# Optimization experiments

Measured on AMD Instinct MI355X. Metric: run time of the kernel, lower is better.

## Reference

```python
import jax, jax.numpy as jnp
import numpy as np

TEMPERATURE = 12.5   # args.temperature (DeepEMD default)
EPS = 0.05           # entropic regularization for the OT (EMD) solve
N_ITERS = 100        # Sinkhorn iterations
COS_EPS = 1e-8       # F.cosine_similarity eps


def setup_inputs() -> dict:
    key = jax.random.key(0)
    k1, k2 = jax.random.split(key)
    B, C, H, W = 512, 1024, 8, 8
    proto = jax.random.normal(k1, (B, C, H, W), dtype=jnp.float32)
    query = jax.random.normal(k2, (B, C, H, W), dtype=jnp.float32)
    return {"proto": proto, "query": query}


def get_weight_vector(A, Bmap):
    """A,[b,c,h,w]; pooled Bmap reweights A's channels -> node weights [b, h*w]."""
    pooled = Bmap.mean(axis=(2, 3), keepdims=True)          # adaptive_avg_pool2d -> [b,c,1,1]
    comb = (A * pooled).sum(axis=1).reshape(A.shape[0], -1)  # [b, h*w]
    return jax.nn.relu(comb) + 0.001


def center(x):
    # args.norm == 'center': subtract channel mean
    return x - x.mean(axis=1, keepdims=True)


def cosine_sim_map(proto, query):
    """sim[b, q_node, p_node] = cosine similarity between flattened spatial nodes."""
    B, C = proto.shape[0], proto.shape[1]
    p = proto.reshape(B, C, -1).transpose(0, 2, 1)   # [b, Np, c]
    q = query.reshape(B, C, -1).transpose(0, 2, 1)   # [b, Nq, c]
    pn = p / jnp.maximum(jnp.linalg.norm(p, axis=-1, keepdims=True), COS_EPS)
    qn = q / jnp.maximum(jnp.linalg.norm(q, axis=-1, keepdims=True), COS_EPS)
    return jnp.einsum('bqc,bpc->bqp', qn, pn)        # [b, Nq, Np]


def sinkhorn_flow(cost, r, c):
    """Entropic-regularized OT flow with marginals r [b,N], c [b,M]; cost [b,N,M]."""
    K = jnp.exp(-cost / EPS)
    v0 = jnp.ones_like(c)

    def body(v, _):
        u = r / jnp.maximum(jnp.einsum('bnm,bm->bn', K, v), 1e-30)
        v = c / jnp.maximum(jnp.einsum('bnm,bn->bm', K, u), 1e-30)
        return v, None

    v, _ = jax.lax.scan(body, v0, None, length=N_ITERS)
    u = r / jnp.maximum(jnp.einsum('bnm,bm->bn', K, v), 1e-30)
    return u[:, :, None] * K * v[:, None, :]         # [b, N, M]


def reference(proto, query):
    # emd_forward(proto, query)
    weight_1 = get_weight_vector(query, proto)       # [b, Nq]
    weight_2 = get_weight_vector(proto, query)       # [b, Np]
    p = center(proto)
    q = center(query)
    sim = cosine_sim_map(p, q)                       # [b, Nq, Np]
    # get_emd_distance: solve OT on cost = 1 - sim with (normalized) node weights
    r = weight_1 / weight_1.sum(axis=-1, keepdims=True)
    c = weight_2 / weight_2.sum(axis=-1, keepdims=True)
    flow = sinkhorn_flow(1.0 - sim, r, c)
    num_node = weight_1.shape[-1]
    logits = (sim * flow).sum(axis=(-1, -2)) * (TEMPERATURE / num_node)
    return logits
```

## Files before the change

### kernel.cpp

```cpp
#include <hip/hip_runtime.h>
#include <math.h>

#define NCH    1024
#define NN     64
#define CK     32
#define KSC    28.853900817779268f
#define SPLIT  4
#define WSB    4352

#define STAT_Q(v) { sqp[0]+=(v).x; q2p[0]=fmaf((v).x,(v).x,q2p[0]); \
                    sqp[1]+=(v).y; q2p[1]=fmaf((v).y,(v).y,q2p[1]); \
                    sqp[2]+=(v).z; q2p[2]=fmaf((v).z,(v).z,q2p[2]); \
                    sqp[3]+=(v).w; q2p[3]=fmaf((v).w,(v).w,q2p[3]); }
#define STAT_P(v) { spp[0]+=(v).x; p2p[0]=fmaf((v).x,(v).x,p2p[0]); \
                    spp[1]+=(v).y; p2p[1]=fmaf((v).y,(v).y,p2p[1]); \
                    spp[2]+=(v).z; p2p[2]=fmaf((v).z,(v).z,p2p[2]); \
                    spp[3]+=(v).w; p2p[3]=fmaf((v).w,(v).w,p2p[3]); }

#define GRAM_CHUNK_BODY(NCHUNK_, QB_, PB_)                                     \
    for (int ch = 0; ch < (NCHUNK_); ++ch) {                                   \
        if (ch) __syncthreads();                                               \
        *(float4*)&stage[       ofs] = qv0;                                    \
        *(float4*)&stage[1024 + ofs] = qv1;                                    \
        *(float4*)&stage[2048 + ofs] = pv0;                                    \
        *(float4*)&stage[3072 + ofs] = pv1;                                    \
        float4 nq0, nq1, np0, np1;                                             \
        const bool more = (ch + 1 < (NCHUNK_));                                \
        if (more) {                                                            \
            const float* qn = (QB_) + (ch + 1) * 2048;                         \
            const float* pn = (PB_) + (ch + 1) * 2048;                         \
            nq0 = *(const float4*)(qn + ofs);                                  \
            nq1 = *(const float4*)(qn + 1024 + ofs);                           \
            np0 = *(const float4*)(pn + ofs);                                  \
            np1 = *(const float4*)(pn + 1024 + ofs);                           \
        }                                                                      \
        STAT_Q(qv0); STAT_Q(qv1);                                              \
        STAT_P(pv0); STAT_P(pv1);                                              \
        __syncthreads();                                                       \
        _Pragma("unroll 8")                                                    \
        for (int cc = 0; cc < CK; ++cc) {                                      \
            float4 a  = *(const float4*)&stage[cc * 64 + n0];                  \
            float4 bb = *(const float4*)&stage[2048 + cc * 64 + m0];           \
            acc[0][0]=fmaf(a.x,bb.x,acc[0][0]); acc[0][1]=fmaf(a.x,bb.y,acc[0][1]); \
            acc[0][2]=fmaf(a.x,bb.z,acc[0][2]); acc[0][3]=fmaf(a.x,bb.w,acc[0][3]); \
            acc[1][0]=fmaf(a.y,bb.x,acc[1][0]); acc[1][1]=fmaf(a.y,bb.y,acc[1][1]); \
            acc[1][2]=fmaf(a.y,bb.z,acc[1][2]); acc[1][3]=fmaf(a.y,bb.w,acc[1][3]); \
            acc[2][0]=fmaf(a.z,bb.x,acc[2][0]); acc[2][1]=fmaf(a.z,bb.y,acc[2][1]); \
            acc[2][2]=fmaf(a.z,bb.z,acc[2][2]); acc[2][3]=fmaf(a.z,bb.w,acc[2][3]); \
            acc[3][0]=fmaf(a.w,bb.x,acc[3][0]); acc[3][1]=fmaf(a.w,bb.y,acc[3][1]); \
            acc[3][2]=fmaf(a.w,bb.z,acc[3][2]); acc[3][3]=fmaf(a.w,bb.w,acc[3][3]); \
        }                                                                      \
        if (more) { qv0 = nq0; qv1 = nq1; pv0 = np0; pv1 = np1; }              \
    }

#define DOT16(KK, ARR) ({ \
    float4 x0 = *(const float4*)&ARR[sp4*16 +  0]; \
    float4 x1 = *(const float4*)&ARR[sp4*16 +  4]; \
    float4 x2 = *(const float4*)&ARR[sp4*16 +  8]; \
    float4 x3 = *(const float4*)&ARR[sp4*16 + 12]; \
    float a0 = 0.0f, a1 = 0.0f; \
    a0=fmaf(KK[0],x0.x,a0);  a1=fmaf(KK[1],x0.y,a1); \
    a0=fmaf(KK[2],x0.z,a0);  a1=fmaf(KK[3],x0.w,a1); \
    a0=fmaf(KK[4],x1.x,a0);  a1=fmaf(KK[5],x1.y,a1); \
    a0=fmaf(KK[6],x1.z,a0);  a1=fmaf(KK[7],x1.w,a1); \
    a0=fmaf(KK[8],x2.x,a0);  a1=fmaf(KK[9],x2.y,a1); \
    a0=fmaf(KK[10],x2.z,a0); a1=fmaf(KK[11],x2.w,a1); \
    a0=fmaf(KK[12],x3.x,a0); a1=fmaf(KK[13],x3.y,a1); \
    a0=fmaf(KK[14],x3.z,a0); a1=fmaf(KK[15],x3.w,a1); \
    a0 + a1; })

__global__ __launch_bounds__(256)
void gram_partial(const float* __restrict__ proto,
                  const float* __restrict__ query,
                  float* __restrict__ ws)
{
    __shared__ __align__(16) float stage[4096];

    const int bid = blockIdx.x;
    const int b = bid >> 2, s = bid & (SPLIT - 1);
    const int t  = threadIdx.x;
    const int tr = t >> 4, tc = t & 15;
    const int n0 = tr * 4, m0 = tc * 4;
    const int ofs = 4 * t;

    const float* __restrict__ pb = proto + (size_t)b * (NCH * NN) + s * (NCH / SPLIT) * NN;
    const float* __restrict__ qb = query + (size_t)b * (NCH * NN) + s * (NCH / SPLIT) * NN;

    float acc[4][4];
    #pragma unroll
    for (int i = 0; i < 4; ++i)
        #pragma unroll
        for (int j = 0; j < 4; ++j) acc[i][j] = 0.0f;
    float sqp[4] = {0,0,0,0}, q2p[4] = {0,0,0,0};
    float spp[4] = {0,0,0,0}, p2p[4] = {0,0,0,0};

    float4 qv0 = *(const float4*)(qb + ofs);
    float4 qv1 = *(const float4*)(qb + 1024 + ofs);
    float4 pv0 = *(const float4*)(pb + ofs);
    float4 pv1 = *(const float4*)(pb + 1024 + ofs);

    GRAM_CHUNK_BODY(NCH / SPLIT / CK, qb, pb)
    __syncthreads();

    float* __restrict__ wsb = ws + (size_t)bid * WSB;
    #pragma unroll
    for (int i = 0; i < 4; ++i) {
        float4 v; v.x = acc[i][0]; v.y = acc[i][1]; v.z = acc[i][2]; v.w = acc[i][3];
        *(float4*)&wsb[(n0 + i) * 64 + m0] = v;
    }

    #pragma unroll
    for (int k = 0; k < 4; ++k) {
        stage[t*16 +      k] = sqp[k];
        stage[t*16 +  4 + k] = q2p[k];
        stage[t*16 +  8 + k] = spp[k];
        stage[t*16 + 12 + k] = p2p[k];
    }
    __syncthreads();
    if (t < NN) {
        const int g = t >> 2, k = t & 3;
        float ssq = 0, sq2 = 0, ssp = 0, sp2 = 0;
        #pragma unroll
        for (int j = 0; j < 16; ++j) {
            const float* row = &stage[(j * 16 + g) * 16];
            ssq += row[k]; sq2 += row[4 + k]; ssp += row[8 + k]; sp2 += row[12 + k];
        }
        wsb[4096 +   0 + t] = ssq;
        wsb[4096 +  64 + t] = sq2;
        wsb[4096 + 128 + t] = ssp;
        wsb[4096 + 192 + t] = sp2;
    }
}

__global__ __launch_bounds__(256)
void emd_solve(const float* __restrict__ ws, float* __restrict__ out)
{
    __shared__ __align__(16) float stage[16 * 64];
    __shared__ __align__(16) float Kl [NN][68];
    __shared__ __align__(16) float KTl[NN][68];
    __shared__ __align__(16) float statL[4][NN];
    __shared__ __align__(16) float uL[NN];
    __shared__ __align__(16) float vL[NN];
    __shared__ __align__(16) float rL[NN];
    __shared__ __align__(16) float cL[NN];
    __shared__ float redl[4];

    const int b  = blockIdx.x;
    const int t  = threadIdx.x;
    const int tr = t >> 4, tc = t & 15;
    const int n0 = tr * 4, m0 = tc * 4;

    const float* __restrict__ wsb = ws + (size_t)b * SPLIT * WSB;

    float acc[4][4];
    #pragma unroll
    for (int i = 0; i < 4; ++i)
        #pragma unroll
        for (int j = 0; j < 4; ++j) acc[i][j] = 0.0f;
    #pragma unroll
    for (int s = 0; s < SPLIT; ++s) {
        const float* __restrict__ g = wsb + s * WSB;
        #pragma unroll
        for (int i = 0; i < 4; ++i) {
            float4 v = *(const float4*)&g[(n0 + i) * 64 + m0];
            acc[i][0] += v.x; acc[i][1] += v.y; acc[i][2] += v.z; acc[i][3] += v.w;
        }
    }
    if (t < NN) {
        float s0 = 0, s1 = 0, s2 = 0, s3 = 0;
        #pragma unroll
        for (int s = 0; s < SPLIT; ++s) {
            const float* __restrict__ g = wsb + s * WSB + 4096;
            s0 += g[t]; s1 += g[64 + t]; s2 += g[128 + t]; s3 += g[192 + t];
        }
        statL[0][t] = s0; statL[1][t] = s1; statL[2][t] = s2; statL[3][t] = s3;
    }
    #pragma unroll
    for (int i = 0; i < 4; ++i) {
        float s = acc[i][0] + acc[i][1] + acc[i][2] + acc[i][3];
        s += __shfl_xor(s, 1, 64); s += __shfl_xor(s, 2, 64);
        s += __shfl_xor(s, 4, 64); s += __shfl_xor(s, 8, 64);
        if (tc == 0) uL[n0 + i] = s;
    }
    #pragma unroll
    for (int j = 0; j < 4; ++j)
        stage[tr * 64 + m0 + j] = acc[0][j] + acc[1][j] + acc[2][j] + acc[3][j];
    __syncthreads();

    if (t < NN) {
        float cs = 0;
        #pragma unroll
        for (int i = 0; i < 16; ++i) cs += stage[i * 64 + t];
        float w2 = fmaxf(cs * (1.0f/64.0f), 0.0f) + 0.001f;
        float w1 = fmaxf(uL[t] * (1.0f/64.0f), 0.0f) + 0.001f;
        float s1 = w1, s2 = w2;
        #pragma unroll
        for (int m = 1; m < 64; m <<= 1) {
            s1 += __shfl_xor(s1, m, 64);
            s2 += __shfl_xor(s2, m, 64);
        }
        rL[t] = w1 / s1;
        cL[t] = w2 / s2;
        vL[t] = 1.0f;
    }
    {
        float nq_[4], np_[4], sqn[4], spm[4];
        #pragma unroll
        for (int i = 0; i < 4; ++i) {
            float sv  = statL[0][n0 + i];
            float var = statL[1][n0 + i] - sv * sv * (1.0f/1024.0f);
            nq_[i] = fmaxf(sqrtf(fmaxf(var, 0.0f)), 1e-8f);
            sqn[i] = sv;
        }
        #pragma unroll
        for (int j = 0; j < 4; ++j) {
            float sv  = statL[2][m0 + j];
            float var = statL[3][m0 + j] - sv * sv * (1.0f/1024.0f);
            np_[j] = fmaxf(sqrtf(fmaxf(var, 0.0f)), 1e-8f);
            spm[j] = sv;
        }
        #pragma unroll
        for (int i = 0; i < 4; ++i) {
            #pragma unroll
            for (int j = 0; j < 4; ++j) {
                float sim = (acc[i][j] - sqn[i] * spm[j] * (1.0f/1024.0f)) / (nq_[i] * np_[j]);
                acc[i][j] = sim;
                float Kv = exp2f((sim - 1.0f) * KSC);
                Kl [n0 + i][m0 + j] = Kv;
                KTl[m0 + j][n0 + i] = Kv;
            }
        }
    }
    __syncthreads();

    const int sn  = t >> 2;
    const int sp4 = t & 3;
    float Kr[16], KTr[16];
    #pragma unroll
    for (int jj = 0; jj < 4; ++jj) {
        float4 kv = *(const float4*)&Kl [sn][sp4 * 16 + jj * 4];
        float4 kt = *(const float4*)&KTl[sn][sp4 * 16 + jj * 4];
        Kr [jj*4+0]=kv.x; Kr [jj*4+1]=kv.y; Kr [jj*4+2]=kv.z; Kr [jj*4+3]=kv.w;
        KTr[jj*4+0]=kt.x; KTr[jj*4+1]=kt.y; KTr[jj*4+2]=kt.z; KTr[jj*4+3]=kt.w;
    }
    const float rreg = rL[sn];
    const float creg = cL[sn];

    for (int it = 0; it < 100; ++it) {
        float s = DOT16(Kr, vL);
        s += __shfl_xor(s, 1, 64); s += __shfl_xor(s, 2, 64);
        float u = rreg / fmaxf(s, 1e-30f);
        if (sp4 == 0) uL[sn] = u;
        __syncthreads();
        float s2 = DOT16(KTr, uL);
        s2 += __shfl_xor(s2, 1, 64); s2 += __shfl_xor(s2, 2, 64);
        float vv = creg / fmaxf(s2, 1e-30f);
        if (sp4 == 0) vL[sn] = vv;
        __syncthreads();
    }
    {
        float s = DOT16(Kr, vL);
        s += __shfl_xor(s, 1, 64); s += __shfl_xor(s, 2, 64);
        float u = rreg / fmaxf(s, 1e-30f);
        if (sp4 == 0) uL[sn] = u;
    }
    __syncthreads();

    float uu[4], vv_[4];
    #pragma unroll
    for (int i = 0; i < 4; ++i) uu[i]  = uL[n0 + i];
    #pragma unroll
    for (int j = 0; j < 4; ++j) vv_[j] = vL[m0 + j];
    float part = 0.0f;
    #pragma unroll
    for (int i = 0; i < 4; ++i) {
        #pragma unroll
        for (int j = 0; j < 4; ++j) {
            float sim = acc[i][j];
            float Kv  = exp2f((sim - 1.0f) * KSC);
            part = fmaf(sim * Kv, uu[i] * vv_[j], part);
        }
    }
    #pragma unroll
    for (int m = 1; m < 64; m <<= 1) part += __shfl_xor(part, m, 64);
    if ((t & 63) == 0) redl[t >> 6] = part;
    __syncthreads();
    if (t == 0) out[b] = (redl[0] + redl[1] + redl[2] + redl[3]) * (12.5f / 64.0f);
}

__global__ __launch_bounds__(256)
void deepemd_fused(const float* __restrict__ proto,
                   const float* __restrict__ query,
                   float* __restrict__ out)
{
    __shared__ __align__(16) float stage[2 * CK * NN];
    __shared__ __align__(16) float Kl [NN][68];
    __shared__ __align__(16) float KTl[NN][68];
    __shared__ __align__(16) float statL[4][NN];
    __shared__ __align__(16) float uL[NN];
    __shared__ __align__(16) float vL[NN];
    __shared__ __align__(16) float rL[NN];
    __shared__ __align__(16) float cL[NN];
    __shared__ float redl[4];

    const int b  = blockIdx.x;
    const int t  = threadIdx.x;
    const int tr = t >> 4, tc = t & 15;
    const int n0 = tr * 4, m0 = tc * 4;
    const int ofs = 4 * t;

    const float* __restrict__ pb = proto + (size_t)b * (NCH * NN);
    const float* __restrict__ qb = query + (size_t)b * (NCH * NN);

    float acc[4][4];
    #pragma unroll
    for (int i = 0; i < 4; ++i)
        #pragma unroll
        for (int j = 0; j < 4; ++j) acc[i][j] = 0.0f;
    float sqp[4] = {0,0,0,0}, q2p[4] = {0,0,0,0};
    float spp[4] = {0,0,0,0}, p2p[4] = {0,0,0,0};

    float4 qv0 = *(const float4*)(qb + ofs);
    float4 qv1 = *(const float4*)(qb + 1024 + ofs);
    float4 pv0 = *(const float4*)(pb + ofs);
    float4 pv1 = *(const float4*)(pb + 1024 + ofs);

    GRAM_CHUNK_BODY(NCH / CK, qb, pb)
    __syncthreads();

    #pragma unroll
    for (int i = 0; i < 4; ++i) {
        float s = acc[i][0] + acc[i][1] + acc[i][2] + acc[i][3];
        s += __shfl_xor(s, 1, 64); s += __shfl_xor(s, 2, 64);
        s += __shfl_xor(s, 4, 64); s += __shfl_xor(s, 8, 64);
        if (tc == 0) uL[n0 + i] = s;
    }
    #pragma unroll
    for (int k = 0; k < 4; ++k) {
        stage[t*16 +      k] = sqp[k];
        stage[t*16 +  4 + k] = q2p[k];
        stage[t*16 +  8 + k] = spp[k];
        stage[t*16 + 12 + k] = p2p[k];
    }
    __syncthreads();
    if (t < NN) {
        const int g = t >> 2, k = t & 3;
        float ssq = 0, sq2 = 0, ssp = 0, sp2 = 0;
        #pragma unroll
        for (int j = 0; j < 16; ++j) {
            const float* row = &stage[(j * 16 + g) * 16];
            ssq += row[k]; sq2 += row[4 + k]; ssp += row[8 + k]; sp2 += row[12 + k];
        }
        statL[0][t] = ssq; statL[1][t] = sq2; statL[2][t] = ssp; statL[3][t] = sp2;
    }
    __syncthreads();
    #pragma unroll
    for (int j = 0; j < 4; ++j)
        stage[tr * 64 + m0 + j] = acc[0][j] + acc[1][j] + acc[2][j] + acc[3][j];
    __syncthreads();
    if (t < NN) {
        float cs = 0;
        #pragma unroll
        for (int i = 0; i < 16; ++i) cs += stage[i * 64 + t];
        float w2 = fmaxf(cs * (1.0f/64.0f), 0.0f) + 0.001f;
        float w1 = fmaxf(uL[t] * (1.0f/64.0f), 0.0f) + 0.001f;
        float s1 = w1, s2 = w2;
        #pragma unroll
        for (int m = 1; m < 64; m <<= 1) {
            s1 += __shfl_xor(s1, m, 64);
            s2 += __shfl_xor(s2, m, 64);
        }
        rL[t] = w1 / s1;
        cL[t] = w2 / s2;
        vL[t] = 1.0f;
    }
    __syncthreads();

    {
        float nq_[4], np_[4], sqn[4], spm[4];
        #pragma unroll
        for (int i = 0; i < 4; ++i) {
            float sv  = statL[0][n0 + i];
            float var = statL[1][n0 + i] - sv * sv * (1.0f/1024.0f);
            nq_[i] = fmaxf(sqrtf(fmaxf(var, 0.0f)), 1e-8f);
            sqn[i] = sv;
        }
        #pragma unroll
        for (int j = 0; j < 4; ++j) {
            float sv  = statL[2][m0 + j];
            float var = statL[3][m0 + j] - sv * sv * (1.0f/1024.0f);
            np_[j] = fmaxf(sqrtf(fmaxf(var, 0.0f)), 1e-8f);
            spm[j] = sv;
        }
        #pragma unroll
        for (int i = 0; i < 4; ++i) {
            #pragma unroll
            for (int j = 0; j < 4; ++j) {
                float sim = (acc[i][j] - sqn[i] * spm[j] * (1.0f/1024.0f)) / (nq_[i] * np_[j]);
                acc[i][j] = sim;
                float Kv = exp2f((sim - 1.0f) * KSC);
                Kl [n0 + i][m0 + j] = Kv;
                KTl[m0 + j][n0 + i] = Kv;
            }
        }
    }
    __syncthreads();

    const int sn  = t >> 2;
    const int sp4 = t & 3;
    float Kr[16], KTr[16];
    #pragma unroll
    for (int jj = 0; jj < 4; ++jj) {
        float4 kv = *(const float4*)&Kl [sn][sp4 * 16 + jj * 4];
        float4 kt = *(const float4*)&KTl[sn][sp4 * 16 + jj * 4];
        Kr [jj*4+0]=kv.x; Kr [jj*4+1]=kv.y; Kr [jj*4+2]=kv.z; Kr [jj*4+3]=kv.w;
        KTr[jj*4+0]=kt.x; KTr[jj*4+1]=kt.y; KTr[jj*4+2]=kt.z; KTr[jj*4+3]=kt.w;
    }
    const float rreg = rL[sn];
    const float creg = cL[sn];

    for (int it = 0; it < 100; ++it) {
        float s = DOT16(Kr, vL);
        s += __shfl_xor(s, 1, 64); s += __shfl_xor(s, 2, 64);
        float u = rreg / fmaxf(s, 1e-30f);
        if (sp4 == 0) uL[sn] = u;
        __syncthreads();
        float s2 = DOT16(KTr, uL);
        s2 += __shfl_xor(s2, 1, 64); s2 += __shfl_xor(s2, 2, 64);
        float vv = creg / fmaxf(s2, 1e-30f);
        if (sp4 == 0) vL[sn] = vv;
        __syncthreads();
    }
    {
        float s = DOT16(Kr, vL);
        s += __shfl_xor(s, 1, 64); s += __shfl_xor(s, 2, 64);
        float u = rreg / fmaxf(s, 1e-30f);
        if (sp4 == 0) uL[sn] = u;
    }
    __syncthreads();

    float uu[4], vv_[4];
    #pragma unroll
    for (int i = 0; i < 4; ++i) uu[i]  = uL[n0 + i];
    #pragma unroll
    for (int j = 0; j < 4; ++j) vv_[j] = vL[m0 + j];
    float part = 0.0f;
    #pragma unroll
    for (int i = 0; i < 4; ++i) {
        #pragma unroll
        for (int j = 0; j < 4; ++j) {
            float sim = acc[i][j];
            float Kv  = exp2f((sim - 1.0f) * KSC);
            part = fmaf(sim * Kv, uu[i] * vv_[j], part);
        }
    }
    #pragma unroll
    for (int m = 1; m < 64; m <<= 1) part += __shfl_xor(part, m, 64);
    if ((t & 63) == 0) redl[t >> 6] = part;
    __syncthreads();
    if (t == 0) out[b] = (redl[0] + redl[1] + redl[2] + redl[3]) * (12.5f / 64.0f);
}

extern "C" void kernel_launch(void* const* d_in, const int* in_sizes, int n_in,
                              void* d_out, int out_size, void* d_ws, size_t ws_size,
                              hipStream_t stream) {
    const float* proto = (const float*)d_in[0];
    const float* query = (const float*)d_in[1];
    float* out = (float*)d_out;
    (void)in_sizes; (void)n_in; (void)out_size;

    const size_t need = (size_t)512 * SPLIT * WSB * sizeof(float);
    if (ws_size >= need) {
        gram_partial<<<dim3(512 * SPLIT), dim3(256), 0, stream>>>(proto, query, (float*)d_ws);
        emd_solve  <<<dim3(512),         dim3(256), 0, stream>>>((const float*)d_ws, out);
    } else {
        deepemd_fused<<<dim3(512), dim3(256), 0, stream>>>(proto, query, out);
    }
}
```

Baseline: 134.5 us.

## Replace gram partial kernel with per-wave streamed global-to-LDS pipelined Gram

The new Gram kernel has each wave independently stream its own 64-channel slice through a double-buffered LDS region, using direct global-to-LDS loads tracked with vmcnt waits instead of block-wide barriers per chunk. Each lane computes an 8x8 register tile over all channels, and the four waves' partial tiles and channel statistics are then reduced sequentially through LDS before one write to the workspace. The aim is to hide HBM latency and drop per-chunk block synchronisation in a memory-bound phase. The larger accumulator and a launch bound requesting four blocks per SM raise register pressure, and the serial cross-wave reduction adds some tail cost. emd_solve is only moved within the file.

```diff
diff --git a/kernel.cpp b/kernel.cpp
--- a/kernel.cpp
+++ b/kernel.cpp
@@ -7,6 +7,329 @@
 #define KSC    28.853900817779268f
 #define SPLIT  4
 #define WSB    4352
+
+__global__ __launch_bounds__(256, 4)
+void gram_stream(const float* __restrict__ proto,
+                 const float* __restrict__ query,
+                 float* __restrict__ ws)
+{
+    __shared__ __align__(16) float lds[4096];
+    __shared__ __align__(16) float statd[4][NN];
+
+    const int bid = blockIdx.x;
+    const int b = bid >> 2, s = bid & 3;
+    const int t = threadIdx.x;
+    const int w = t >> 6;
+    const int l = t & 63;
+    const int r0 = (l >> 3) * 8;
+    const int c0 = (l & 7) * 8;
+
+    const float* __restrict__ qw = query + (size_t)b * (NCH * NN) + (s * 256 + w * 64) * NN;
+    const float* __restrict__ pw = proto + (size_t)b * (NCH * NN) + (s * 256 + w * 64) * NN;
+
+    float* const stg = &lds[w * 1024];
+
+    float acc[8][8];
+    #pragma unroll
+    for (int i = 0; i < 8; ++i)
+        #pragma unroll
+        for (int j = 0; j < 8; ++j) acc[i][j] = 0.0f;
+    float sqa[8] = {0,0,0,0,0,0,0,0}, q2a[8] = {0,0,0,0,0,0,0,0};
+    float spb[8] = {0,0,0,0,0,0,0,0}, p2b[8] = {0,0,0,0,0,0,0,0};
+
+#define ISSUE(CH) do {                                                          \
+        const int kb_ = (CH) & 1;                                               \
+        const float* gq_ = qw + (CH) * 256 + 4 * l;                             \
+        const float* gp_ = pw + (CH) * 256 + 4 * l;                             \
+        __builtin_amdgcn_global_load_lds(                                       \
+            (const __attribute__((address_space(1))) void*)gq_,                 \
+            (__attribute__((address_space(3))) void*)(stg + kb_ * 512), 16, 0, 0); \
+        __builtin_amdgcn_global_load_lds(                                       \
+            (const __attribute__((address_space(1))) void*)gp_,                 \
+            (__attribute__((address_space(3))) void*)(stg + kb_ * 512 + 256), 16, 0, 0); \
+    } while (0)
+
+#define COMPUTE(CH) do {                                                        \
+        const float* sq_ = stg + ((CH) & 1) * 512;                              \
+        const float* sp_ = sq_ + 256;                                           \
+        _Pragma("unroll")                                                       \
+        for (int cc = 0; cc < 4; ++cc) {                                        \
+            float4 a0 = *(const float4*)(sq_ + cc * 64 + r0);                   \
+            float4 a1 = *(const float4*)(sq_ + cc * 64 + r0 + 4);               \
+            float4 b0 = *(const float4*)(sp_ + cc * 64 + c0);                   \
+            float4 b1 = *(const float4*)(sp_ + cc * 64 + c0 + 4);               \
+            const float av[8] = {a0.x,a0.y,a0.z,a0.w,a1.x,a1.y,a1.z,a1.w};      \
+            const float bv[8] = {b0.x,b0.y,b0.z,b0.w,b1.x,b1.y,b1.z,b1.w};      \
+            _Pragma("unroll")                                                   \
+            for (int i = 0; i < 8; ++i) {                                       \
+                sqa[i] += av[i]; q2a[i] = fmaf(av[i], av[i], q2a[i]);           \
+                spb[i] += bv[i]; p2b[i] = fmaf(bv[i], bv[i], p2b[i]);           \
+            }                                                                   \
+            _Pragma("unroll")                                                   \
+            for (int i = 0; i < 8; ++i)                                         \
+                _Pragma("unroll")                                               \
+                for (int j = 0; j < 8; ++j)                                     \
+                    acc[i][j] = fmaf(av[i], bv[j], acc[i][j]);                  \
+        }                                                                       \
+    } while (0)
+
+    ISSUE(0);
+    ISSUE(1);
+
+    for (int ch = 0; ch < 15; ++ch) {
+        asm volatile("s_waitcnt vmcnt(2)" ::: "memory");
+        __builtin_amdgcn_sched_barrier(0);
+        COMPUTE(ch);
+        if (ch + 2 < 16) ISSUE(ch + 2);
+    }
+    asm volatile("s_waitcnt vmcnt(0)" ::: "memory");
+    __builtin_amdgcn_sched_barrier(0);
+    COMPUTE(15);
+
+    __syncthreads();
+
+    float* __restrict__ wsb = ws + (size_t)bid * WSB;
+
+    #pragma unroll 1
+    for (int wv = 0; wv < 4; ++wv) {
+        if (w == wv) {
+            if (wv == 0) {
+                #pragma unroll
+                for (int i = 0; i < 8; ++i) {
+                    float4 v0; v0.x=acc[i][0]; v0.y=acc[i][1]; v0.z=acc[i][2]; v0.w=acc[i][3];
+                    float4 v1; v1.x=acc[i][4]; v1.y=acc[i][5]; v1.z=acc[i][6]; v1.w=acc[i][7];
+                    *(float4*)&lds[(r0 + i) * 64 + c0]     = v0;
+                    *(float4*)&lds[(r0 + i) * 64 + c0 + 4] = v1;
+                }
+                if ((l & 7) == 0) {
+                    #pragma unroll
+                    for (int i = 0; i < 8; ++i) { statd[0][r0 + i] = sqa[i]; statd[1][r0 + i] = q2a[i]; }
+                }
+                if (l < 8) {
+                    #pragma unroll
+                    for (int j = 0; j < 8; ++j) { statd[2][c0 + j] = spb[j]; statd[3][c0 + j] = p2b[j]; }
+                }
+            } else if (wv < 3) {
+                #pragma unroll
+                for (int i = 0; i < 8; ++i) {
+                    float4 d0 = *(const float4*)&lds[(r0 + i) * 64 + c0];
+                    float4 d1 = *(const float4*)&lds[(r0 + i) * 64 + c0 + 4];
+                    d0.x+=acc[i][0]; d0.y+=acc[i][1]; d0.z+=acc[i][2]; d0.w+=acc[i][3];
+                    d1.x+=acc[i][4]; d1.y+=acc[i][5]; d1.z+=acc[i][6]; d1.w+=acc[i][7];
+                    *(float4*)&lds[(r0 + i) * 64 + c0]     = d0;
+                    *(float4*)&lds[(r0 + i) * 64 + c0 + 4] = d1;
+                }
+                if ((l & 7) == 0) {
+                    #pragma unroll
+                    for (int i = 0; i < 8; ++i) { statd[0][r0 + i] += sqa[i]; statd[1][r0 + i] += q2a[i]; }
+                }
+                if (l < 8) {
+                    #pragma unroll
+                    for (int j = 0; j < 8; ++j) { statd[2][c0 + j] += spb[j]; statd[3][c0 + j] += p2b[j]; }
+                }
+            } else {
+                #pragma unroll
+                for (int i = 0; i < 8; ++i) {
+                    float4 d0 = *(const float4*)&lds[(r0 + i) * 64 + c0];
+                    float4 d1 = *(const float4*)&lds[(r0 + i) * 64 + c0 + 4];
+                    d0.x+=acc[i][0]; d0.y+=acc[i][1]; d0.z+=acc[i][2]; d0.w+=acc[i][3];
+                    d1.x+=acc[i][4]; d1.y+=acc[i][5]; d1.z+=acc[i][6]; d1.w+=acc[i][7];
+                    *(float4*)&wsb[(r0 + i) * 64 + c0]     = d0;
+                    *(float4*)&wsb[(r0 + i) * 64 + c0 + 4] = d1;
+                }
+                if ((l & 7) == 0) {
+                    #pragma unroll
+                    for (int i = 0; i < 8; ++i) {
+                        wsb[4096 +   0 + r0 + i] = statd[0][r0 + i] + sqa[i];
+                        wsb[4096 +  64 + r0 + i] = statd[1][r0 + i] + q2a[i];
+                    }
+                }
+                if (l < 8) {
+                    #pragma unroll
+                    for (int j = 0; j < 8; ++j) {
+                        wsb[4096 + 128 + c0 + j] = statd[2][c0 + j] + spb[j];
+                        wsb[4096 + 192 + c0 + j] = statd[3][c0 + j] + p2b[j];
+                    }
+                }
+            }
+        }
+        if (wv < 3) __syncthreads();
+    }
+#undef ISSUE
+#undef COMPUTE
+}
+
+#define DOT16(KK, ARR) ({ \
+    float4 x0 = *(const float4*)&ARR[sp4*16 +  0]; \
+    float4 x1 = *(const float4*)&ARR[sp4*16 +  4]; \
+    float4 x2 = *(const float4*)&ARR[sp4*16 +  8]; \
+    float4 x3 = *(const float4*)&ARR[sp4*16 + 12]; \
+    float a0 = 0.0f, a1 = 0.0f; \
+    a0=fmaf(KK[0],x0.x,a0);  a1=fmaf(KK[1],x0.y,a1); \
+    a0=fmaf(KK[2],x0.z,a0);  a1=fmaf(KK[3],x0.w,a1); \
+    a0=fmaf(KK[4],x1.x,a0);  a1=fmaf(KK[5],x1.y,a1); \
+    a0=fmaf(KK[6],x1.z,a0);  a1=fmaf(KK[7],x1.w,a1); \
+    a0=fmaf(KK[8],x2.x,a0);  a1=fmaf(KK[9],x2.y,a1); \
+    a0=fmaf(KK[10],x2.z,a0); a1=fmaf(KK[11],x2.w,a1); \
+    a0=fmaf(KK[12],x3.x,a0); a1=fmaf(KK[13],x3.y,a1); \
+    a0=fmaf(KK[14],x3.z,a0); a1=fmaf(KK[15],x3.w,a1); \
+    a0 + a1; })
+
+__global__ __launch_bounds__(256)
+void emd_solve(const float* __restrict__ ws, float* __restrict__ out)
+{
+    __shared__ __align__(16) float stage[16 * 64];
+    __shared__ __align__(16) float Kl [NN][68];
+    __shared__ __align__(16) float KTl[NN][68];
+    __shared__ __align__(16) float statL[4][NN];
+    __shared__ __align__(16) float uL[NN];
+    __shared__ __align__(16) float vL[NN];
+    __shared__ __align__(16) float rL[NN];
+    __shared__ __align__(16) float cL[NN];
+    __shared__ float redl[4];
+
+    const int b  = blockIdx.x;
+    const int t  = threadIdx.x;
+    const int tr = t >> 4, tc = t & 15;
+    const int n0 = tr * 4, m0 = tc * 4;
+
+    const float* __restrict__ wsb = ws + (size_t)b * SPLIT * WSB;
+
+    float acc[4][4];
+    #pragma unroll
+    for (int i = 0; i < 4; ++i)
+        #pragma unroll
+        for (int j = 0; j < 4; ++j) acc[i][j] = 0.0f;
+    #pragma unroll
+    for (int s = 0; s < SPLIT; ++s) {
+        const float* __restrict__ g = wsb + s * WSB;
+        #pragma unroll
+        for (int i = 0; i < 4; ++i) {
+            float4 v = *(const float4*)&g[(n0 + i) * 64 + m0];
+            acc[i][0] += v.x; acc[i][1] += v.y; acc[i][2] += v.z; acc[i][3] += v.w;
+        }
+    }
+    if (t < NN) {
+        float s0 = 0, s1 = 0, s2 = 0, s3 = 0;
+        #pragma unroll
+        for (int s = 0; s < SPLIT; ++s) {
+            const float* __restrict__ g = wsb + s * WSB + 4096;
+            s0 += g[t]; s1 += g[64 + t]; s2 += g[128 + t]; s3 += g[192 + t];
+        }
+        statL[0][t] = s0; statL[1][t] = s1; statL[2][t] = s2; statL[3][t] = s3;
+    }
+    #pragma unroll
+    for (int i = 0; i < 4; ++i) {
+        float s = acc[i][0] + acc[i][1] + acc[i][2] + acc[i][3];
+        s += __shfl_xor(s, 1, 64); s += __shfl_xor(s, 2, 64);
+        s += __shfl_xor(s, 4, 64); s += __shfl_xor(s, 8, 64);
+        if (tc == 0) uL[n0 + i] = s;
+    }
+    #pragma unroll
+    for (int j = 0; j < 4; ++j)
+        stage[tr * 64 + m0 + j] = acc[0][j] + acc[1][j] + acc[2][j] + acc[3][j];
+    __syncthreads();
+
+    if (t < NN) {
+        float cs = 0;
+        #pragma unroll
+        for (int i = 0; i < 16; ++i) cs += stage[i * 64 + t];
+        float w2 = fmaxf(cs * (1.0f/64.0f), 0.0f) + 0.001f;
+        float w1 = fmaxf(uL[t] * (1.0f/64.0f), 0.0f) + 0.001f;
+        float s1 = w1, s2 = w2;
+        #pragma unroll
+        for (int m = 1; m < 64; m <<= 1) {
+            s1 += __shfl_xor(s1, m, 64);
+            s2 += __shfl_xor(s2, m, 64);
+        }
+        rL[t] = w1 / s1;
+        cL[t] = w2 / s2;
+        vL[t] = 1.0f;
+    }
+    {
+        float nq_[4], np_[4], sqn[4], spm[4];
+        #pragma unroll
+        for (int i = 0; i < 4; ++i) {
+            float sv  = statL[0][n0 + i];
+            float var = statL[1][n0 + i] - sv * sv * (1.0f/1024.0f);
+            nq_[i] = fmaxf(sqrtf(fmaxf(var, 0.0f)), 1e-8f);
+            sqn[i] = sv;
+        }
+        #pragma unroll
+        for (int j = 0; j < 4; ++j) {
+            float sv  = statL[2][m0 + j];
+            float var = statL[3][m0 + j] - sv * sv * (1.0f/1024.0f);
+            np_[j] = fmaxf(sqrtf(fmaxf(var, 0.0f)), 1e-8f);
+            spm[j] = sv;
+        }
+        #pragma unroll
+        for (int i = 0; i < 4; ++i) {
+            #pragma unroll
+            for (int j = 0; j < 4; ++j) {
+                float sim = (acc[i][j] - sqn[i] * spm[j] * (1.0f/1024.0f)) / (nq_[i] * np_[j]);
+                acc[i][j] = sim;
+                float Kv = exp2f((sim - 1.0f) * KSC);
+                Kl [n0 + i][m0 + j] = Kv;
+                KTl[m0 + j][n0 + i] = Kv;
+            }
+        }
+    }
+    __syncthreads();
+
+    const int sn  = t >> 2;
+    const int sp4 = t & 3;
+    float Kr[16], KTr[16];
+    #pragma unroll
+    for (int jj = 0; jj < 4; ++jj) {
+        float4 kv = *(const float4*)&Kl [sn][sp4 * 16 + jj * 4];
+        float4 kt = *(const float4*)&KTl[sn][sp4 * 16 + jj * 4];
+        Kr [jj*4+0]=kv.x; Kr [jj*4+1]=kv.y; Kr [jj*4+2]=kv.z; Kr [jj*4+3]=kv.w;
+        KTr[jj*4+0]=kt.x; KTr[jj*4+1]=kt.y; KTr[jj*4+2]=kt.z; KTr[jj*4+3]=kt.w;
+    }
+    const float rreg = rL[sn];
+    const float creg = cL[sn];
+
+    for (int it = 0; it < 100; ++it) {
+        float s = DOT16(Kr, vL);
+        s += __shfl_xor(s, 1, 64); s += __shfl_xor(s, 2, 64);
+        float u = rreg / fmaxf(s, 1e-30f);
+        if (sp4 == 0) uL[sn] = u;
+        __syncthreads();
+        float s2 = DOT16(KTr, uL);
+        s2 += __shfl_xor(s2, 1, 64); s2 += __shfl_xor(s2, 2, 64);
+        float vv = creg / fmaxf(s2, 1e-30f);
+        if (sp4 == 0) vL[sn] = vv;
+        __syncthreads();
+    }
+    {
+        float s = DOT16(Kr, vL);
+        s += __shfl_xor(s, 1, 64); s += __shfl_xor(s, 2, 64);
+        float u = rreg / fmaxf(s, 1e-30f);
+        if (sp4 == 0) uL[sn] = u;
+    }
+    __syncthreads();
+
+    float uu[4], vv_[4];
+    #pragma unroll
+    for (int i = 0; i < 4; ++i) uu[i]  = uL[n0 + i];
+    #pragma unroll
+    for (int j = 0; j < 4; ++j) vv_[j] = vL[m0 + j];
+    float part = 0.0f;
+    #pragma unroll
+    for (int i = 0; i < 4; ++i) {
+        #pragma unroll
+        for (int j = 0; j < 4; ++j) {
+            float sim = acc[i][j];
+            float Kv  = exp2f((sim - 1.0f) * KSC);
+            part = fmaf(sim * Kv, uu[i] * vv_[j], part);
+        }
+    }
+    #pragma unroll
+    for (int m = 1; m < 64; m <<= 1) part += __shfl_xor(part, m, 64);
+    if ((t & 63) == 0) redl[t >> 6] = part;
+    __syncthreads();
+    if (t == 0) out[b] = (redl[0] + redl[1] + redl[2] + redl[3]) * (12.5f / 64.0f);
+}
 
 #define STAT_Q(v) { sqp[0]+=(v).x; q2p[0]=fmaf((v).x,(v).x,q2p[0]); \
                     sqp[1]+=(v).y; q2p[1]=fmaf((v).y,(v).y,q2p[1]); \
@@ -53,241 +376,6 @@
         if (more) { qv0 = nq0; qv1 = nq1; pv0 = np0; pv1 = np1; }              \
     }
 
-#define DOT16(KK, ARR) ({ \
-    float4 x0 = *(const float4*)&ARR[sp4*16 +  0]; \
-    float4 x1 = *(const float4*)&ARR[sp4*16 +  4]; \
-    float4 x2 = *(const float4*)&ARR[sp4*16 +  8]; \
-    float4 x3 = *(const float4*)&ARR[sp4*16 + 12]; \
-    float a0 = 0.0f, a1 = 0.0f; \
-    a0=fmaf(KK[0],x0.x,a0);  a1=fmaf(KK[1],x0.y,a1); \
-    a0=fmaf(KK[2],x0.z,a0);  a1=fmaf(KK[3],x0.w,a1); \
-    a0=fmaf(KK[4],x1.x,a0);  a1=fmaf(KK[5],x1.y,a1); \
-    a0=fmaf(KK[6],x1.z,a0);  a1=fmaf(KK[7],x1.w,a1); \
-    a0=fmaf(KK[8],x2.x,a0);  a1=fmaf(KK[9],x2.y,a1); \
-    a0=fmaf(KK[10],x2.z,a0); a1=fmaf(KK[11],x2.w,a1); \
-    a0=fmaf(KK[12],x3.x,a0); a1=fmaf(KK[13],x3.y,a1); \
-    a0=fmaf(KK[14],x3.z,a0); a1=fmaf(KK[15],x3.w,a1); \
-    a0 + a1; })
-
-__global__ __launch_bounds__(256)
-void gram_partial(const float* __restrict__ proto,
-                  const float* __restrict__ query,
-                  float* __restrict__ ws)
-{
-    __shared__ __align__(16) float stage[4096];
-
-    const int bid = blockIdx.x;
-    const int b = bid >> 2, s = bid & (SPLIT - 1);
-    const int t  = threadIdx.x;
-    const int tr = t >> 4, tc = t & 15;
-    const int n0 = tr * 4, m0 = tc * 4;
-    const int ofs = 4 * t;
-
-    const float* __restrict__ pb = proto + (size_t)b * (NCH * NN) + s * (NCH / SPLIT) * NN;
-    const float* __restrict__ qb = query + (size_t)b * (NCH * NN) + s * (NCH / SPLIT) * NN;
-
-    float acc[4][4];
-    #pragma unroll
-    for (int i = 0; i < 4; ++i)
-        #pragma unroll
-        for (int j = 0; j < 4; ++j) acc[i][j] = 0.0f;
-    float sqp[4] = {0,0,0,0}, q2p[4] = {0,0,0,0};
-    float spp[4] = {0,0,0,0}, p2p[4] = {0,0,0,0};
-
-    float4 qv0 = *(const float4*)(qb + ofs);
-    float4 qv1 = *(const float4*)(qb + 1024 + ofs);
-    float4 pv0 = *(const float4*)(pb + ofs);
-    float4 pv1 = *(const float4*)(pb + 1024 + ofs);
-
-    GRAM_CHUNK_BODY(NCH / SPLIT / CK, qb, pb)
-    __syncthreads();
-
-    float* __restrict__ wsb = ws + (size_t)bid * WSB;
-    #pragma unroll
-    for (int i = 0; i < 4; ++i) {
-        float4 v; v.x = acc[i][0]; v.y = acc[i][1]; v.z = acc[i][2]; v.w = acc[i][3];
-        *(float4*)&wsb[(n0 + i) * 64 + m0] = v;
-    }
-
-    #pragma unroll
-    for (int k = 0; k < 4; ++k) {
-        stage[t*16 +      k] = sqp[k];
-        stage[t*16 +  4 + k] = q2p[k];
-        stage[t*16 +  8 + k] = spp[k];
-        stage[t*16 + 12 + k] = p2p[k];
-    }
-    __syncthreads();
-    if (t < NN) {
-        const int g = t >> 2, k = t & 3;
-        float ssq = 0, sq2 = 0, ssp = 0, sp2 = 0;
-        #pragma unroll
-        for (int j = 0; j < 16; ++j) {
-            const float* row = &stage[(j * 16 + g) * 16];
-            ssq += row[k]; sq2 += row[4 + k]; ssp += row[8 + k]; sp2 += row[12 + k];
-        }
-        wsb[4096 +   0 + t] = ssq;
-        wsb[4096 +  64 + t] = sq2;
-        wsb[4096 + 128 + t] = ssp;
-        wsb[4096 + 192 + t] = sp2;
-    }
-}
-
-__global__ __launch_bounds__(256)
-void emd_solve(const float* __restrict__ ws, float* __restrict__ out)
-{
-    __shared__ __align__(16) float stage[16 * 64];
-    __shared__ __align__(16) float Kl [NN][68];
-    __shared__ __align__(16) float KTl[NN][68];
-    __shared__ __align__(16) float statL[4][NN];
-    __shared__ __align__(16) float uL[NN];
-    __shared__ __align__(16) float vL[NN];
-    __shared__ __align__(16) float rL[NN];
-    __shared__ __align__(16) float cL[NN];
-    __shared__ float redl[4];
-
-    const int b  = blockIdx.x;
-    const int t  = threadIdx.x;
-    const int tr = t >> 4, tc = t & 15;
-    const int n0 = tr * 4, m0 = tc * 4;
-
-    const float* __restrict__ wsb = ws + (size_t)b * SPLIT * WSB;
-
-    float acc[4][4];
-    #pragma unroll
-    for (int i = 0; i < 4; ++i)
-        #pragma unroll
-        for (int j = 0; j < 4; ++j) acc[i][j] = 0.0f;
-    #pragma unroll
-    for (int s = 0; s < SPLIT; ++s) {
-        const float* __restrict__ g = wsb + s * WSB;
-        #pragma unroll
-        for (int i = 0; i < 4; ++i) {
-            float4 v = *(const float4*)&g[(n0 + i) * 64 + m0];
-            acc[i][0] += v.x; acc[i][1] += v.y; acc[i][2] += v.z; acc[i][3] += v.w;
-        }
-    }
-    if (t < NN) {
-        float s0 = 0, s1 = 0, s2 = 0, s3 = 0;
-        #pragma unroll
-        for (int s = 0; s < SPLIT; ++s) {
-            const float* __restrict__ g = wsb + s * WSB + 4096;
-            s0 += g[t]; s1 += g[64 + t]; s2 += g[128 + t]; s3 += g[192 + t];
-        }
-        statL[0][t] = s0; statL[1][t] = s1; statL[2][t] = s2; statL[3][t] = s3;
-    }
-    #pragma unroll
-    for (int i = 0; i < 4; ++i) {
-        float s = acc[i][0] + acc[i][1] + acc[i][2] + acc[i][3];
-        s += __shfl_xor(s, 1, 64); s += __shfl_xor(s, 2, 64);
-        s += __shfl_xor(s, 4, 64); s += __shfl_xor(s, 8, 64);
-        if (tc == 0) uL[n0 + i] = s;
-    }
-    #pragma unroll
-    for (int j = 0; j < 4; ++j)
-        stage[tr * 64 + m0 + j] = acc[0][j] + acc[1][j] + acc[2][j] + acc[3][j];
-    __syncthreads();
-
-    if (t < NN) {
-        float cs = 0;
-        #pragma unroll
-        for (int i = 0; i < 16; ++i) cs += stage[i * 64 + t];
-        float w2 = fmaxf(cs * (1.0f/64.0f), 0.0f) + 0.001f;
-        float w1 = fmaxf(uL[t] * (1.0f/64.0f), 0.0f) + 0.001f;
-        float s1 = w1, s2 = w2;
-        #pragma unroll
-        for (int m = 1; m < 64; m <<= 1) {
-            s1 += __shfl_xor(s1, m, 64);
-            s2 += __shfl_xor(s2, m, 64);
-        }
-        rL[t] = w1 / s1;
-        cL[t] = w2 / s2;
-        vL[t] = 1.0f;
-    }
-    {
-        float nq_[4], np_[4], sqn[4], spm[4];
-        #pragma unroll
-        for (int i = 0; i < 4; ++i) {
-            float sv  = statL[0][n0 + i];
-            float var = statL[1][n0 + i] - sv * sv * (1.0f/1024.0f);
-            nq_[i] = fmaxf(sqrtf(fmaxf(var, 0.0f)), 1e-8f);
-            sqn[i] = sv;
-        }
-        #pragma unroll
-        for (int j = 0; j < 4; ++j) {
-            float sv  = statL[2][m0 + j];
-            float var = statL[3][m0 + j] - sv * sv * (1.0f/1024.0f);
-            np_[j] = fmaxf(sqrtf(fmaxf(var, 0.0f)), 1e-8f);
-            spm[j] = sv;
-        }
-        #pragma unroll
-        for (int i = 0; i < 4; ++i) {
-            #pragma unroll
-            for (int j = 0; j < 4; ++j) {
-                float sim = (acc[i][j] - sqn[i] * spm[j] * (1.0f/1024.0f)) / (nq_[i] * np_[j]);
-                acc[i][j] = sim;
-                float Kv = exp2f((sim - 1.0f) * KSC);
-                Kl [n0 + i][m0 + j] = Kv;
-                KTl[m0 + j][n0 + i] = Kv;
-            }
-        }
-    }
-    __syncthreads();
-
-    const int sn  = t >> 2;
-    const int sp4 = t & 3;
-    float Kr[16], KTr[16];
-    #pragma unroll
-    for (int jj = 0; jj < 4; ++jj) {
-        float4 kv = *(const float4*)&Kl [sn][sp4 * 16 + jj * 4];
-        float4 kt = *(const float4*)&KTl[sn][sp4 * 16 + jj * 4];
-        Kr [jj*4+0]=kv.x; Kr [jj*4+1]=kv.y; Kr [jj*4+2]=kv.z; Kr [jj*4+3]=kv.w;
-        KTr[jj*4+0]=kt.x; KTr[jj*4+1]=kt.y; KTr[jj*4+2]=kt.z; KTr[jj*4+3]=kt.w;
-    }
-    const float rreg = rL[sn];
-    const float creg = cL[sn];
-
-    for (int it = 0; it < 100; ++it) {
-        float s = DOT16(Kr, vL);
-        s += __shfl_xor(s, 1, 64); s += __shfl_xor(s, 2, 64);
-        float u = rreg / fmaxf(s, 1e-30f);
-        if (sp4 == 0) uL[sn] = u;
-        __syncthreads();
-        float s2 = DOT16(KTr, uL);
-        s2 += __shfl_xor(s2, 1, 64); s2 += __shfl_xor(s2, 2, 64);
-        float vv = creg / fmaxf(s2, 1e-30f);
-        if (sp4 == 0) vL[sn] = vv;
-        __syncthreads();
-    }
-    {
-        float s = DOT16(Kr, vL);
-        s += __shfl_xor(s, 1, 64); s += __shfl_xor(s, 2, 64);
-        float u = rreg / fmaxf(s, 1e-30f);
-        if (sp4 == 0) uL[sn] = u;
-    }
-    __syncthreads();
-
-    float uu[4], vv_[4];
-    #pragma unroll
-    for (int i = 0; i < 4; ++i) uu[i]  = uL[n0 + i];
-    #pragma unroll
-    for (int j = 0; j < 4; ++j) vv_[j] = vL[m0 + j];
-    float part = 0.0f;
-    #pragma unroll
-    for (int i = 0; i < 4; ++i) {
-        #pragma unroll
-        for (int j = 0; j < 4; ++j) {
-            float sim = acc[i][j];
-            float Kv  = exp2f((sim - 1.0f) * KSC);
-            part = fmaf(sim * Kv, uu[i] * vv_[j], part);
-        }
-    }
-    #pragma unroll
-    for (int m = 1; m < 64; m <<= 1) part += __shfl_xor(part, m, 64);
-    if ((t & 63) == 0) redl[t >> 6] = part;
-    __syncthreads();
-    if (t == 0) out[b] = (redl[0] + redl[1] + redl[2] + redl[3]) * (12.5f / 64.0f);
-}
-
 __global__ __launch_bounds__(256)
 void deepemd_fused(const float* __restrict__ proto,
                    const float* __restrict__ query,
@@ -471,7 +559,7 @@
 
     const size_t need = (size_t)512 * SPLIT * WSB * sizeof(float);
     if (ws_size >= need) {
-        gram_partial<<<dim3(512 * SPLIT), dim3(256), 0, stream>>>(proto, query, (float*)d_ws);
+        gram_stream<<<dim3(512 * SPLIT), dim3(256), 0, stream>>>(proto, query, (float*)d_ws);
         emd_solve  <<<dim3(512),         dim3(256), 0, stream>>>((const float*)d_ws, out);
     } else {
         deepemd_fused<<<dim3(512), dim3(256), 0, stream>>>(proto, query, out);
```

Result: slower. 200.4 us (+49.0%).
